# Performance work log

Measured on AMD Instinct MI355X. Metric: run time of the kernel, lower is better.

The kernel has to match this reference:

```python
import jax, jax.numpy as jnp
import numpy as np

L, H = 16384, 1024

def setup_inputs() -> dict:
    key = jax.random.key(0)
    x = jax.random.normal(key, (L, H), dtype=jnp.float32)
    # learned parameter: tau initialized to log(0.8) per channel
    tau = jnp.full((H,), jnp.log(jnp.float32(0.8)), dtype=jnp.float32)
    return {"x": x, "tau": tau}

def _binop(q_i, q_j):
    # diagonal linear recurrence combine: x_j = A_j * x_i + b_j
    A_i, b_i = q_i
    A_j, b_j = q_j
    return (A_j * A_i, A_j * b_i + b_j)

def reference(x, tau):
    # Lambda_bar = exp(tau), B_bar = I  => Bu_elements = x
    Lambda_bar = jnp.exp(tau)                         # (H,)
    B_bar = jnp.eye(x.shape[1], dtype=x.dtype)        # (H, H) identity, as in original
    Bu = jnp.einsum('ph,lh->lp', B_bar, x)            # (L, H) == x
    Lambda_elements = jnp.broadcast_to(Lambda_bar, x.shape)  # (L, H)
    _, xs = jax.lax.associative_scan(_binop, (Lambda_elements, Bu))
    return xs  # (L, H)
```

## Files before the change

### kernel.cpp

```cpp
#include <hip/hip_runtime.h>
#include <hip/hip_cooperative_groups.h>
#include <cmath>


namespace cg = cooperative_groups;

static constexpr int TC = 16;
static constexpr int P  = 16;

typedef float nt4 __attribute__((ext_vector_type(4)));

__device__ inline float4 ntload(const float4* p) {
    nt4 v = __builtin_nontemporal_load((const nt4*)p);
    return make_float4(v.x, v.y, v.z, v.w);
}

__global__ __launch_bounds__(256, 4)
void li_coop(const float4* __restrict__ xv, const float4* __restrict__ tauv,
             float4* __restrict__ yv, float4* __restrict__ ends,
             float4* __restrict__ pa, int HV, int NP)
{
    const int t = threadIdx.x;
    const int c = blockIdx.x;

    const float4 tv = tauv[t];
    const float lx = expf(tv.x), ly = expf(tv.y),
                lz = expf(tv.z), lw = expf(tv.w);
    const float Tx = expf(tv.x * (float)TC), Ty = expf(tv.y * (float)TC),
                Tz = expf(tv.z * (float)TC), Tw = expf(tv.w * (float)TC);
    const float fQ = (float)(TC * P);
    const float Qx = expf(tv.x * fQ), Qy = expf(tv.y * fQ),
                Qz = expf(tv.z * fQ), Qw = expf(tv.w * fQ);

    const size_t base = (size_t)c * TC * HV + t;
    float4 buf[TC];
#pragma unroll
    for (int i = 0; i < TC; ++i)
        buf[i] = ntload(&xv[base + (size_t)i * HV]);

    float4 s = make_float4(0.f, 0.f, 0.f, 0.f);
#pragma unroll
    for (int i = 0; i < TC; ++i) {
        s.x = fmaf(lx, s.x, buf[i].x);
        s.y = fmaf(ly, s.y, buf[i].y);
        s.z = fmaf(lz, s.z, buf[i].z);
        s.w = fmaf(lw, s.w, buf[i].w);
        buf[i] = s;
    }
    ends[(size_t)c * HV + t] = s;

    cg::this_grid().sync();

    if (c < NP) {
        const float4* ep = ends + (size_t)c * P * HV + t;
        float4 a = make_float4(0.f, 0.f, 0.f, 0.f);
#pragma unroll
        for (int j0 = 0; j0 < P; j0 += 8) {
            float4 v[8];
#pragma unroll
            for (int j = 0; j < 8; ++j)
                v[j] = ep[(size_t)(j0 + j) * HV];
#pragma unroll
            for (int j = 0; j < 8; ++j) {
                a.x = fmaf(Tx, a.x, v[j].x);
                a.y = fmaf(Ty, a.y, v[j].y);
                a.z = fmaf(Tz, a.z, v[j].z);
                a.w = fmaf(Tw, a.w, v[j].w);
            }
        }
        pa[(size_t)c * HV + t] = a;
    }

    cg::this_grid().sync();

    const int p = c / P;
    const int r = c % P;

    float4 carry = make_float4(0.f, 0.f, 0.f, 0.f);
    for (int q0 = 0; q0 < p; q0 += 8) {
        const int n = p - q0;
        float4 v[8];
#pragma unroll
        for (int j = 0; j < 8; ++j)
            if (j < n) v[j] = pa[(size_t)(q0 + j) * HV + t];
#pragma unroll
        for (int j = 0; j < 8; ++j) {
            if (j < n) {
                carry.x = fmaf(Qx, carry.x, v[j].x);
                carry.y = fmaf(Qy, carry.y, v[j].y);
                carry.z = fmaf(Qz, carry.z, v[j].z);
                carry.w = fmaf(Qw, carry.w, v[j].w);
            }
        }
    }
    {
        const float4* ep = ends + (size_t)p * P * HV + t;
        for (int j0 = 0; j0 < r; j0 += 8) {
            const int n = r - j0;
            float4 v[8];
#pragma unroll
            for (int j = 0; j < 8; ++j)
                if (j < n) v[j] = ep[(size_t)(j0 + j) * HV];
#pragma unroll
            for (int j = 0; j < 8; ++j) {
                if (j < n) {
                    carry.x = fmaf(Tx, carry.x, v[j].x);
                    carry.y = fmaf(Ty, carry.y, v[j].y);
                    carry.z = fmaf(Tz, carry.z, v[j].z);
                    carry.w = fmaf(Tw, carry.w, v[j].w);
                }
            }
        }
    }

    float4 pm = make_float4(lx, ly, lz, lw);
    nt4* yn = (nt4*)yv;
#pragma unroll
    for (int i = 0; i < TC; ++i) {
        nt4 o = { fmaf(pm.x, carry.x, buf[i].x),
                  fmaf(pm.y, carry.y, buf[i].y),
                  fmaf(pm.z, carry.z, buf[i].z),
                  fmaf(pm.w, carry.w, buf[i].w) };
        __builtin_nontemporal_store(o, &yn[base + (size_t)i * HV]);
        pm.x *= lx; pm.y *= ly; pm.z *= lz; pm.w *= lw;
    }
}


__global__ __launch_bounds__(256)
void li_ends(const float4* __restrict__ xv, const float4* __restrict__ tauv,
             float4* __restrict__ ends, int HV) {
    const int t = threadIdx.x;
    const int c = blockIdx.x;
    const float4 tv = tauv[t];
    const float lx = expf(tv.x), ly = expf(tv.y),
                lz = expf(tv.z), lw = expf(tv.w);
    const float4* xp = xv + (size_t)c * TC * HV + t;
    float4 buf[TC];
#pragma unroll
    for (int i = 0; i < TC; ++i)
        buf[i] = xp[(size_t)i * HV];
    float4 s = make_float4(0.f, 0.f, 0.f, 0.f);
#pragma unroll
    for (int i = 0; i < TC; ++i) {
        s.x = fmaf(lx, s.x, buf[i].x);
        s.y = fmaf(ly, s.y, buf[i].y);
        s.z = fmaf(lz, s.z, buf[i].z);
        s.w = fmaf(lw, s.w, buf[i].w);
    }
    ends[(size_t)c * HV + t] = s;
}

__global__ __launch_bounds__(256)
void li_pagg(const float4* __restrict__ ends, const float4* __restrict__ tauv,
             float4* __restrict__ pa, int HV) {
    const int gid = blockIdx.x * 256 + threadIdx.x;
    const int t = gid % HV;
    const int p = gid / HV;
    const float4 tv = tauv[t];
    const float Tx = expf(tv.x * (float)TC), Ty = expf(tv.y * (float)TC),
                Tz = expf(tv.z * (float)TC), Tw = expf(tv.w * (float)TC);
    const float4* ep = ends + (size_t)p * P * HV + t;
    float4 buf[P];
#pragma unroll
    for (int j = 0; j < P; ++j)
        buf[j] = ep[(size_t)j * HV];
    float4 s = make_float4(0.f, 0.f, 0.f, 0.f);
#pragma unroll
    for (int j = 0; j < P; ++j) {
        s.x = fmaf(Tx, s.x, buf[j].x);
        s.y = fmaf(Ty, s.y, buf[j].y);
        s.z = fmaf(Tz, s.z, buf[j].z);
        s.w = fmaf(Tw, s.w, buf[j].w);
    }
    pa[(size_t)p * HV + t] = s;
}

__global__ __launch_bounds__(256)
void li_pscan(float4* __restrict__ pa, const float4* __restrict__ tauv,
              int HV, int NP) {
    const int t = threadIdx.x;
    const float4 tv = tauv[t];
    const float fP = (float)(P * TC);
    const float Px = expf(tv.x * fP), Py = expf(tv.y * fP),
                Pz = expf(tv.z * fP), Pw = expf(tv.w * fP);
    float4 c = make_float4(0.f, 0.f, 0.f, 0.f);
    for (int p0 = 0; p0 < NP; p0 += 16) {
        float4 v[16];
#pragma unroll
        for (int j = 0; j < 16; ++j)
            v[j] = pa[(size_t)(p0 + j) * HV + t];
#pragma unroll
        for (int j = 0; j < 16; ++j) {
            const float4 a = v[j];
            v[j] = c;
            c.x = fmaf(Px, c.x, a.x);
            c.y = fmaf(Py, c.y, a.y);
            c.z = fmaf(Pz, c.z, a.z);
            c.w = fmaf(Pw, c.w, a.w);
        }
#pragma unroll
        for (int j = 0; j < 16; ++j)
            pa[(size_t)(p0 + j) * HV + t] = v[j];
    }
}

__global__ __launch_bounds__(256)
void li_out(const float4* __restrict__ xv, const float4* __restrict__ tauv,
            const float4* __restrict__ ends, const float4* __restrict__ pc,
            float4* __restrict__ yv, int HV) {
    const int t = threadIdx.x;
    const int c = blockIdx.x;
    const int p = c / P;
    const int r = c % P;
    const float4 tv = tauv[t];
    const float lx = expf(tv.x), ly = expf(tv.y),
                lz = expf(tv.z), lw = expf(tv.w);
    const float Tx = expf(tv.x * (float)TC), Ty = expf(tv.y * (float)TC),
                Tz = expf(tv.z * (float)TC), Tw = expf(tv.w * (float)TC);
    float4 carry = pc[(size_t)p * HV + t];
    {
        float4 v[P - 1];
        const float4* ep = ends + (size_t)p * P * HV + t;
#pragma unroll
        for (int j = 0; j < P - 1; ++j)
            if (j < r) v[j] = ep[(size_t)j * HV];
#pragma unroll
        for (int j = 0; j < P - 1; ++j) {
            if (j < r) {
                carry.x = fmaf(Tx, carry.x, v[j].x);
                carry.y = fmaf(Ty, carry.y, v[j].y);
                carry.z = fmaf(Tz, carry.z, v[j].z);
                carry.w = fmaf(Tw, carry.w, v[j].w);
            }
        }
    }
    const size_t base = (size_t)c * TC * HV + t;
    float4 buf[TC];
#pragma unroll
    for (int i = 0; i < TC; ++i)
        buf[i] = xv[base + (size_t)i * HV];
    float4 s = carry;
#pragma unroll
    for (int i = 0; i < TC; ++i) {
        s.x = fmaf(lx, s.x, buf[i].x);
        s.y = fmaf(ly, s.y, buf[i].y);
        s.z = fmaf(lz, s.z, buf[i].z);
        s.w = fmaf(lw, s.w, buf[i].w);
        buf[i] = s;
    }
    nt4* yn = (nt4*)yv;
#pragma unroll
    for (int i = 0; i < TC; ++i) {
        nt4 o = { buf[i].x, buf[i].y, buf[i].z, buf[i].w };
        __builtin_nontemporal_store(o, &yn[base + (size_t)i * HV]);
    }
}

extern "C" void kernel_launch(void* const* d_in, const int* in_sizes, int n_in,
                              void* d_out, int out_size, void* d_ws, size_t ws_size,
                              hipStream_t stream) {
    const float* x   = (const float*)d_in[0];
    const float* tau = (const float*)d_in[1];
    float* y = (float*)d_out;

    const int H  = in_sizes[1];
    const int L  = in_sizes[0] / H;
    const int C  = L / TC;
    const int NP = C / P;
    const int HV = H / 4;

    float4* ends = (float4*)d_ws;
    float4* pa   = ends + (size_t)C * HV;

    const float4* xv   = (const float4*)x;
    const float4* tauv = (const float4*)tau;
    float4*       yv   = (float4*)y;

    int blocksPerCU = 0;
    hipError_t qe = hipOccupancyMaxActiveBlocksPerMultiprocessor(
        &blocksPerCU, li_coop, 256, 0);

    bool coop_ok = false;
    if (qe == hipSuccess && blocksPerCU >= 4) {
        void* args[] = { (void*)&xv, (void*)&tauv, (void*)&yv,
                         (void*)&ends, (void*)&pa, (void*)&HV, (void*)&NP };
        hipError_t le = hipLaunchCooperativeKernel(
            li_coop, dim3(C), dim3(256), args, 0u, stream);
        coop_ok = (le == hipSuccess);
    }

    if (!coop_ok) {
        li_ends <<<dim3(C),             dim3(256), 0, stream>>>(xv, tauv, ends, HV);
        li_pagg <<<dim3(NP * HV / 256), dim3(256), 0, stream>>>(ends, tauv, pa, HV);
        li_pscan<<<dim3(1),             dim3(256), 0, stream>>>(pa, tauv, HV, NP);
        li_out  <<<dim3(C),             dim3(256), 0, stream>>>(xv, tauv, ends, pa,
                                                                yv, HV);
    }
}
```

Before: 132.3 us.

## Replace cooperative grid syncs with flag-based decoupled lookback chunk scan

Adds a single-pass kernel in which each block publishes its chunk end state with a release flag. Blocks within a group of P chunks then wait only on their predecessors' flags instead of grid-wide barriers. The last block of each group computes the group aggregate and a carry over earlier groups, then publishes it for its peers. This removes cooperative-launch grid syncs and their global stalls, at the cost of spin-waiting, a memset of the flags, and reliance on all blocks being co-resident, which is checked against the occupancy query and CU count.

```diff
diff --git a/kernel.cpp b/kernel.cpp
--- a/kernel.cpp
+++ b/kernel.cpp
@@ -7,6 +7,7 @@
 
 static constexpr int TC = 16;
 static constexpr int P  = 16;
+static constexpr int FS = 32;
 
 typedef float nt4 __attribute__((ext_vector_type(4)));
 
@@ -14,6 +15,156 @@
     nt4 v = __builtin_nontemporal_load((const nt4*)p);
     return make_float4(v.x, v.y, v.z, v.w);
 }
+
+__device__ inline unsigned ld_flag(unsigned* p) {
+    return __hip_atomic_load(p, __ATOMIC_RELAXED, __HIP_MEMORY_SCOPE_AGENT);
+}
+__device__ inline void st_flag(unsigned* p, unsigned v) {
+    __hip_atomic_store(p, v, __ATOMIC_RELEASE, __HIP_MEMORY_SCOPE_AGENT);
+}
+
+__global__ __launch_bounds__(256, 4)
+void li_lookback(const float4* __restrict__ xv, const float4* __restrict__ tauv,
+                 float4* __restrict__ yv, float4* __restrict__ ends,
+                 float4* __restrict__ pagg, float4* __restrict__ qc,
+                 unsigned* __restrict__ eflag, unsigned* __restrict__ aflag,
+                 unsigned* __restrict__ qflag, int HV)
+{
+    const int t = threadIdx.x;
+    const int c = blockIdx.x;
+    const int p = c / P;
+    const int r = c % P;
+
+    const float4 tv = tauv[t];
+    const float lx = expf(tv.x), ly = expf(tv.y),
+                lz = expf(tv.z), lw = expf(tv.w);
+    const float Tx = expf(tv.x * (float)TC), Ty = expf(tv.y * (float)TC),
+                Tz = expf(tv.z * (float)TC), Tw = expf(tv.w * (float)TC);
+
+    const size_t base = (size_t)c * TC * HV + t;
+    float4 buf[TC];
+#pragma unroll
+    for (int i = 0; i < TC; ++i)
+        buf[i] = ntload(&xv[base + (size_t)i * HV]);
+
+    float4 s = make_float4(0.f, 0.f, 0.f, 0.f);
+#pragma unroll
+    for (int i = 0; i < TC; ++i) {
+        s.x = fmaf(lx, s.x, buf[i].x);
+        s.y = fmaf(ly, s.y, buf[i].y);
+        s.z = fmaf(lz, s.z, buf[i].z);
+        s.w = fmaf(lw, s.w, buf[i].w);
+        buf[i] = s;
+    }
+    ends[(size_t)c * HV + t] = s;
+    __threadfence();
+    __syncthreads();
+    if (t == 0) st_flag(&eflag[(size_t)c * FS], 1u);
+
+    if (t < r) {
+        while (ld_flag(&eflag[(size_t)(p * P + t) * FS]) == 0u)
+            __builtin_amdgcn_s_sleep(1);
+    }
+    __syncthreads();
+    __threadfence();
+
+    float4 w = make_float4(0.f, 0.f, 0.f, 0.f);
+    const float4* ep = ends + (size_t)p * P * HV + t;
+    for (int j0 = 0; j0 < r; j0 += 4) {
+        float4 v[4];
+#pragma unroll
+        for (int j = 0; j < 4; ++j)
+            if (j0 + j < r) v[j] = ep[(size_t)(j0 + j) * HV];
+#pragma unroll
+        for (int j = 0; j < 4; ++j) {
+            if (j0 + j < r) {
+                w.x = fmaf(Tx, w.x, v[j].x);
+                w.y = fmaf(Ty, w.y, v[j].y);
+                w.z = fmaf(Tz, w.z, v[j].z);
+                w.w = fmaf(Tw, w.w, v[j].w);
+            }
+        }
+    }
+
+    float4 cc;
+    const float fr = (float)(TC * r);
+    if (r == P - 1) {
+        float4 a;
+        a.x = fmaf(Tx, w.x, s.x);
+        a.y = fmaf(Ty, w.y, s.y);
+        a.z = fmaf(Tz, w.z, s.z);
+        a.w = fmaf(Tw, w.w, s.w);
+        pagg[(size_t)p * HV + t] = a;
+        __threadfence();
+        __syncthreads();
+        if (t == 0) st_flag(&aflag[(size_t)p * FS], 1u);
+
+        if (t < p) {
+            while (ld_flag(&aflag[(size_t)t * FS]) == 0u)
+                __builtin_amdgcn_s_sleep(1);
+        }
+        __syncthreads();
+        __threadfence();
+
+        const float fQ = (float)(TC * P);
+        const float Qx = expf(tv.x * fQ), Qy = expf(tv.y * fQ),
+                    Qz = expf(tv.z * fQ), Qw = expf(tv.w * fQ);
+        float4 carry = make_float4(0.f, 0.f, 0.f, 0.f);
+        for (int q0 = 0; q0 < p; q0 += 4) {
+            float4 v[4];
+#pragma unroll
+            for (int j = 0; j < 4; ++j)
+                if (q0 + j < p) v[j] = pagg[(size_t)(q0 + j) * HV + t];
+#pragma unroll
+            for (int j = 0; j < 4; ++j) {
+                if (q0 + j < p) {
+                    carry.x = fmaf(Qx, carry.x, v[j].x);
+                    carry.y = fmaf(Qy, carry.y, v[j].y);
+                    carry.z = fmaf(Qz, carry.z, v[j].z);
+                    carry.w = fmaf(Qw, carry.w, v[j].w);
+                }
+            }
+        }
+        qc[(size_t)p * HV + t] = carry;
+        __threadfence();
+        __syncthreads();
+        if (t == 0) st_flag(&qflag[(size_t)p * FS], 1u);
+
+        const float Rx = expf(tv.x * fr), Ry = expf(tv.y * fr),
+                    Rz = expf(tv.z * fr), Rw = expf(tv.w * fr);
+        cc.x = fmaf(Rx, carry.x, w.x);
+        cc.y = fmaf(Ry, carry.y, w.y);
+        cc.z = fmaf(Rz, carry.z, w.z);
+        cc.w = fmaf(Rw, carry.w, w.w);
+    } else {
+        if (t == 0) {
+            while (ld_flag(&qflag[(size_t)p * FS]) == 0u)
+                __builtin_amdgcn_s_sleep(1);
+        }
+        __syncthreads();
+        __threadfence();
+        const float4 qv = qc[(size_t)p * HV + t];
+        const float Rx = expf(tv.x * fr), Ry = expf(tv.y * fr),
+                    Rz = expf(tv.z * fr), Rw = expf(tv.w * fr);
+        cc.x = fmaf(Rx, qv.x, w.x);
+        cc.y = fmaf(Ry, qv.y, w.y);
+        cc.z = fmaf(Rz, qv.z, w.z);
+        cc.w = fmaf(Rw, qv.w, w.w);
+    }
+
+    float4 pm = make_float4(lx, ly, lz, lw);
+    nt4* yn = (nt4*)yv;
+#pragma unroll
+    for (int i = 0; i < TC; ++i) {
+        nt4 o = { fmaf(pm.x, cc.x, buf[i].x),
+                  fmaf(pm.y, cc.y, buf[i].y),
+                  fmaf(pm.z, cc.z, buf[i].z),
+                  fmaf(pm.w, cc.w, buf[i].w) };
+        __builtin_nontemporal_store(o, &yn[base + (size_t)i * HV]);
+        pm.x *= lx; pm.y *= ly; pm.z *= lz; pm.w *= lw;
+    }
+}
+
 
 __global__ __launch_bounds__(256, 4)
 void li_coop(const float4* __restrict__ xv, const float4* __restrict__ tauv,
@@ -271,20 +422,50 @@
     const int HV = H / 4;
 
     float4* ends = (float4*)d_ws;
-    float4* pa   = ends + (size_t)C * HV;
+    float4* pagg = ends + (size_t)C * HV;
+    float4* qc   = pagg + (size_t)NP * HV;
+    unsigned* eflag = (unsigned*)(qc + (size_t)NP * HV);
+    unsigned* aflag = eflag + (size_t)C * FS;
+    unsigned* qflag = aflag + (size_t)NP * FS;
+    const size_t flagBytes = (size_t)(C + 2 * NP) * FS * sizeof(unsigned);
+    const size_t needLB = ((size_t)C * HV + 2 * (size_t)NP * HV) * sizeof(float4)
+                          + flagBytes;
 
     const float4* xv   = (const float4*)x;
     const float4* tauv = (const float4*)tau;
     float4*       yv   = (float4*)y;
 
+    static int lb_bpc = -1;
+    static int nCU    = -1;
+    if (lb_bpc < 0) {
+        int b = 0;
+        if (hipOccupancyMaxActiveBlocksPerMultiprocessor(&b, li_lookback, 256, 0)
+            != hipSuccess) b = 0;
+        lb_bpc = b;
+        hipDeviceProp_t prop;
+        int dev = 0;
+        if (hipGetDevice(&dev) == hipSuccess &&
+            hipGetDeviceProperties(&prop, dev) == hipSuccess)
+            nCU = prop.multiProcessorCount;
+        else
+            nCU = 0;
+    }
+
+    if (lb_bpc >= 4 && (size_t)lb_bpc * (size_t)nCU >= (size_t)C &&
+        ws_size >= needLB) {
+        hipMemsetAsync(eflag, 0, flagBytes, stream);
+        li_lookback<<<dim3(C), dim3(256), 0, stream>>>(
+            xv, tauv, yv, ends, pagg, qc, eflag, aflag, qflag, HV);
+        return;
+    }
+
     int blocksPerCU = 0;
     hipError_t qe = hipOccupancyMaxActiveBlocksPerMultiprocessor(
         &blocksPerCU, li_coop, 256, 0);
-
     bool coop_ok = false;
     if (qe == hipSuccess && blocksPerCU >= 4) {
         void* args[] = { (void*)&xv, (void*)&tauv, (void*)&yv,
-                         (void*)&ends, (void*)&pa, (void*)&HV, (void*)&NP };
+                         (void*)&ends, (void*)&pagg, (void*)&HV, (void*)&NP };
         hipError_t le = hipLaunchCooperativeKernel(
             li_coop, dim3(C), dim3(256), args, 0u, stream);
         coop_ok = (le == hipSuccess);
@@ -292,9 +473,9 @@
 
     if (!coop_ok) {
         li_ends <<<dim3(C),             dim3(256), 0, stream>>>(xv, tauv, ends, HV);
-        li_pagg <<<dim3(NP * HV / 256), dim3(256), 0, stream>>>(ends, tauv, pa, HV);
-        li_pscan<<<dim3(1),             dim3(256), 0, stream>>>(pa, tauv, HV, NP);
-        li_out  <<<dim3(C),             dim3(256), 0, stream>>>(xv, tauv, ends, pa,
+        li_pagg <<<dim3(NP * HV / 256), dim3(256), 0, stream>>>(ends, tauv, pagg, HV);
+        li_pscan<<<dim3(1),             dim3(256), 0, stream>>>(pagg, tauv, HV, NP);
+        li_out  <<<dim3(C),             dim3(256), 0, stream>>>(xv, tauv, ends, pagg,
                                                                 yv, HV);
     }
 }
```

Result: no change. 132.7 us (+0.3%).

## Replace cooperative three-phase scan with independent windowed lookback blocks

Applied to the files above, without the earlier changes.

Drops the cooperative kernel and its two grid-wide syncs and ends/partials workspace. Each block now owns 64 rows and rebuilds its incoming carry by rescanning only the previous 64 rows. It falls back to a full prefix rescan when the largest decay is too slow for the window contribution to be negligible (tau*64 > -13.8). The aim is to remove global synchronisation and workspace traffic. The cost is reading x about twice, a truncation error near e^-13.8, and only 256 blocks with a long serial dependent chain per thread.

```diff
diff --git a/kernel.cpp b/kernel.cpp
--- a/kernel.cpp
+++ b/kernel.cpp
@@ -1,128 +1,65 @@
 #include <hip/hip_runtime.h>
-#include <hip/hip_cooperative_groups.h>
 #include <cmath>
 
 
-namespace cg = cooperative_groups;
-
+static constexpr int BR = 64;
+static constexpr int W  = 64;
 static constexpr int TC = 16;
 static constexpr int P  = 16;
 
 typedef float nt4 __attribute__((ext_vector_type(4)));
 
-__device__ inline float4 ntload(const float4* p) {
-    nt4 v = __builtin_nontemporal_load((const nt4*)p);
-    return make_float4(v.x, v.y, v.z, v.w);
-}
-
-__global__ __launch_bounds__(256, 4)
-void li_coop(const float4* __restrict__ xv, const float4* __restrict__ tauv,
-             float4* __restrict__ yv, float4* __restrict__ ends,
-             float4* __restrict__ pa, int HV, int NP)
+__global__ __launch_bounds__(256, 1)
+void li_win(const float4* __restrict__ xv, const float4* __restrict__ tauv,
+            float4* __restrict__ yv, int HV)
 {
     const int t = threadIdx.x;
     const int c = blockIdx.x;
+    const int r0 = c * BR;
 
     const float4 tv = tauv[t];
     const float lx = expf(tv.x), ly = expf(tv.y),
                 lz = expf(tv.z), lw = expf(tv.w);
-    const float Tx = expf(tv.x * (float)TC), Ty = expf(tv.y * (float)TC),
-                Tz = expf(tv.z * (float)TC), Tw = expf(tv.w * (float)TC);
-    const float fQ = (float)(TC * P);
-    const float Qx = expf(tv.x * fQ), Qy = expf(tv.y * fQ),
-                Qz = expf(tv.z * fQ), Qw = expf(tv.w * fQ);
-
-    const size_t base = (size_t)c * TC * HV + t;
-    float4 buf[TC];
-#pragma unroll
-    for (int i = 0; i < TC; ++i)
-        buf[i] = ntload(&xv[base + (size_t)i * HV]);
 
     float4 s = make_float4(0.f, 0.f, 0.f, 0.f);
-#pragma unroll
-    for (int i = 0; i < TC; ++i) {
-        s.x = fmaf(lx, s.x, buf[i].x);
-        s.y = fmaf(ly, s.y, buf[i].y);
-        s.z = fmaf(lz, s.z, buf[i].z);
-        s.w = fmaf(lw, s.w, buf[i].w);
-        buf[i] = s;
-    }
-    ends[(size_t)c * HV + t] = s;
-
-    cg::this_grid().sync();
-
-    if (c < NP) {
-        const float4* ep = ends + (size_t)c * P * HV + t;
-        float4 a = make_float4(0.f, 0.f, 0.f, 0.f);
-#pragma unroll
-        for (int j0 = 0; j0 < P; j0 += 8) {
-            float4 v[8];
-#pragma unroll
-            for (int j = 0; j < 8; ++j)
-                v[j] = ep[(size_t)(j0 + j) * HV];
-#pragma unroll
-            for (int j = 0; j < 8; ++j) {
-                a.x = fmaf(Tx, a.x, v[j].x);
-                a.y = fmaf(Ty, a.y, v[j].y);
-                a.z = fmaf(Tz, a.z, v[j].z);
-                a.w = fmaf(Tw, a.w, v[j].w);
+
+    if (c > 0) {
+        const int rw = r0 - W;
+
+        const float mt = fmaxf(fmaxf(tv.x, tv.y), fmaxf(tv.z, tv.w));
+        if (mt * (float)W > -13.8f) {
+            const float4* xp0 = xv + t;
+            for (int rr = 0; rr < rw; ++rr) {
+                const float4 v = xp0[(size_t)rr * HV];
+                s.x = fmaf(lx, s.x, v.x);
+                s.y = fmaf(ly, s.y, v.y);
+                s.z = fmaf(lz, s.z, v.z);
+                s.w = fmaf(lw, s.w, v.w);
             }
         }
-        pa[(size_t)c * HV + t] = a;
-    }
-
-    cg::this_grid().sync();
-
-    const int p = c / P;
-    const int r = c % P;
-
-    float4 carry = make_float4(0.f, 0.f, 0.f, 0.f);
-    for (int q0 = 0; q0 < p; q0 += 8) {
-        const int n = p - q0;
-        float4 v[8];
-#pragma unroll
-        for (int j = 0; j < 8; ++j)
-            if (j < n) v[j] = pa[(size_t)(q0 + j) * HV + t];
-#pragma unroll
-        for (int j = 0; j < 8; ++j) {
-            if (j < n) {
-                carry.x = fmaf(Qx, carry.x, v[j].x);
-                carry.y = fmaf(Qy, carry.y, v[j].y);
-                carry.z = fmaf(Qz, carry.z, v[j].z);
-                carry.w = fmaf(Qw, carry.w, v[j].w);
-            }
-        }
-    }
-    {
-        const float4* ep = ends + (size_t)p * P * HV + t;
-        for (int j0 = 0; j0 < r; j0 += 8) {
-            const int n = r - j0;
-            float4 v[8];
-#pragma unroll
-            for (int j = 0; j < 8; ++j)
-                if (j < n) v[j] = ep[(size_t)(j0 + j) * HV];
-#pragma unroll
-            for (int j = 0; j < 8; ++j) {
-                if (j < n) {
-                    carry.x = fmaf(Tx, carry.x, v[j].x);
-                    carry.y = fmaf(Ty, carry.y, v[j].y);
-                    carry.z = fmaf(Tz, carry.z, v[j].z);
-                    carry.w = fmaf(Tw, carry.w, v[j].w);
-                }
-            }
-        }
-    }
-
-    float4 pm = make_float4(lx, ly, lz, lw);
-    nt4* yn = (nt4*)yv;
-#pragma unroll
-    for (int i = 0; i < TC; ++i) {
-        nt4 o = { fmaf(pm.x, carry.x, buf[i].x),
-                  fmaf(pm.y, carry.y, buf[i].y),
-                  fmaf(pm.z, carry.z, buf[i].z),
-                  fmaf(pm.w, carry.w, buf[i].w) };
-        __builtin_nontemporal_store(o, &yn[base + (size_t)i * HV]);
-        pm.x *= lx; pm.y *= ly; pm.z *= lz; pm.w *= lw;
+
+        const float4* xp = xv + (size_t)rw * HV + t;
+#pragma unroll
+        for (int i = 0; i < W; ++i) {
+            const float4 v = xp[(size_t)i * HV];
+            s.x = fmaf(lx, s.x, v.x);
+            s.y = fmaf(ly, s.y, v.y);
+            s.z = fmaf(lz, s.z, v.z);
+            s.w = fmaf(lw, s.w, v.w);
+        }
+    }
+
+    const float4* xp = xv + (size_t)r0 * HV + t;
+    nt4* yp = (nt4*)yv + (size_t)r0 * HV + t;
+#pragma unroll
+    for (int i = 0; i < BR; ++i) {
+        const float4 v = xp[(size_t)i * HV];
+        s.x = fmaf(lx, s.x, v.x);
+        s.y = fmaf(ly, s.y, v.y);
+        s.z = fmaf(lz, s.z, v.z);
+        s.w = fmaf(lw, s.w, v.w);
+        nt4 o = { s.x, s.y, s.z, s.w };
+        __builtin_nontemporal_store(o, &yp[(size_t)i * HV]);
     }
 }
 
@@ -266,35 +203,25 @@
 
     const int H  = in_sizes[1];
     const int L  = in_sizes[0] / H;
-    const int C  = L / TC;
-    const int NP = C / P;
     const int HV = H / 4;
-
-    float4* ends = (float4*)d_ws;
-    float4* pa   = ends + (size_t)C * HV;
 
     const float4* xv   = (const float4*)x;
     const float4* tauv = (const float4*)tau;
     float4*       yv   = (float4*)y;
 
-    int blocksPerCU = 0;
-    hipError_t qe = hipOccupancyMaxActiveBlocksPerMultiprocessor(
-        &blocksPerCU, li_coop, 256, 0);
-
-    bool coop_ok = false;
-    if (qe == hipSuccess && blocksPerCU >= 4) {
-        void* args[] = { (void*)&xv, (void*)&tauv, (void*)&yv,
-                         (void*)&ends, (void*)&pa, (void*)&HV, (void*)&NP };
-        hipError_t le = hipLaunchCooperativeKernel(
-            li_coop, dim3(C), dim3(256), args, 0u, stream);
-        coop_ok = (le == hipSuccess);
-    }
-
-    if (!coop_ok) {
-        li_ends <<<dim3(C),             dim3(256), 0, stream>>>(xv, tauv, ends, HV);
-        li_pagg <<<dim3(NP * HV / 256), dim3(256), 0, stream>>>(ends, tauv, pa, HV);
-        li_pscan<<<dim3(1),             dim3(256), 0, stream>>>(pa, tauv, HV, NP);
-        li_out  <<<dim3(C),             dim3(256), 0, stream>>>(xv, tauv, ends, pa,
-                                                                yv, HV);
-    }
-}
+    if (HV == 256 && (L % BR) == 0 && (H % 4) == 0) {
+        li_win<<<dim3(L / BR), dim3(256), 0, stream>>>(xv, tauv, yv, HV);
+        return;
+    }
+
+    const int C  = L / TC;
+    const int NP = C / P;
+    float4* ends = (float4*)d_ws;
+    float4* pa   = ends + (size_t)C * HV;
+
+    li_ends <<<dim3(C),             dim3(256), 0, stream>>>(xv, tauv, ends, HV);
+    li_pagg <<<dim3(NP * HV / 256), dim3(256), 0, stream>>>(ends, tauv, pa, HV);
+    li_pscan<<<dim3(1),             dim3(256), 0, stream>>>(pa, tauv, HV, NP);
+    li_out  <<<dim3(C),             dim3(256), 0, stream>>>(xv, tauv, ends, pa,
+                                                            yv, HV);
+}
```

After: 115.5 us. -12.7%, faster.
